# Performance work log

Measured on AMD Instinct MI355X. Metric: run time of the kernel, lower is better.

Reference implementation:

```python
import jax, jax.numpy as jnp
import numpy as np

N_HEADS = 8

def setup_inputs() -> dict:
    key = jax.random.key(0)
    ks = jax.random.split(key, 7)
    B, S, D = 4, 2048, 512
    s = 1.0 / np.sqrt(D)
    return {
        "input_Q": jax.random.normal(ks[0], (B, S, D), jnp.float32),
        "input_K": jax.random.normal(ks[1], (B, S, D), jnp.float32),
        "input_V": jax.random.normal(ks[2], (B, S, D), jnp.float32),
        "W_Q": jax.random.normal(ks[3], (D, D), jnp.float32) * s,
        "W_K": jax.random.normal(ks[4], (D, D), jnp.float32) * s,
        "W_V": jax.random.normal(ks[5], (D, D), jnp.float32) * s,
        "W_O": jax.random.normal(ks[6], (D, D), jnp.float32) * s,
    }

def reference(input_Q, input_K, input_V, W_Q, W_K, W_V, W_O):
    B, Sq, D = input_Q.shape
    Sk = input_K.shape[1]
    H = N_HEADS
    d_k = D // H
    # torch nn.Linear(bias=False): y = x @ W.T
    def proj(x, W):
        return (x @ W.T).reshape(B, -1, H, d_k).transpose(0, 2, 1, 3)  # [B,H,S,dk]
    Q = proj(input_Q, W_Q)
    K = proj(input_K, W_K)
    V = proj(input_V, W_V)
    scale = 1.0 / jnp.sqrt(jnp.float32(d_k))
    scores = jnp.einsum("bhqd,bhkd->bhqk", Q, K) * scale  # [B,H,Sq,Sk]
    # TriangularCausalMask: mask strict upper triangle with -inf
    causal = jnp.tril(jnp.ones((Sq, Sk), dtype=bool))
    scores = jnp.where(causal[None, None], scores, -jnp.inf)
    attn = jax.nn.softmax(scores, axis=-1)
    context = jnp.einsum("bhqk,bhkd->bhqd", attn, V)
    context = context.transpose(0, 2, 1, 3).reshape(B, Sq, D)
    return context @ W_O.T
```

## Files before the change

### kernel.cpp

```cpp
#include <hip/hip_runtime.h>
#include <hip/hip_bf16.h>
#include <math.h>

#define B_  4
#define S_  2048
#define D_  512
#define H_  8
#define DK_ 64
#define M_  (B_ * S_)

using bf16   = __bf16;
using bf16x4 = __bf16 __attribute__((ext_vector_type(4)));
using bf16x8 = __bf16 __attribute__((ext_vector_type(8)));
using f32x4  = float __attribute__((ext_vector_type(4)));

#define MFMA16(a, b, c) __builtin_amdgcn_mfma_f32_16x16x32_bf16((a), (b), (c), 0, 0, 0)
#define EXP2(x) exp2f(x)

typedef __attribute__((address_space(3))) void       lds_void;
typedef const __attribute__((address_space(1))) void gbl_void;

__device__ __forceinline__ void async16(const bf16* g, bf16* lds) {
    __builtin_amdgcn_global_load_lds((gbl_void*)g, (lds_void*)lds, 16, 0, 0);
}

__device__ __forceinline__ bf16x8 ldg8(const bf16* p) {
    return *reinterpret_cast<const bf16x8*>(p);
}

__device__ __forceinline__ size_t fragbase(int g, int k0, int kk, int t) {
    return ((((size_t)(g * 8 + k0) * 2 + kk) * 4 + t) * 64) * 8;
}

__global__ __launch_bounds__(256) void cvt_all(
    const float* __restrict__ x0, const float* __restrict__ x1, const float* __restrict__ x2,
    const float* __restrict__ w0, const float* __restrict__ w1,
    const float* __restrict__ w2, const float* __restrict__ w3,
    bf16* __restrict__ dst)
{
    const int w    = blockIdx.x * 4 + (threadIdx.x >> 6);
    const int lane = threadIdx.x & 63;
    const int lg = lane >> 4, lc = lane & 15;
    const float* src;
    int c;
    size_t dbase;
    if (w < 24576) {
        const int seg = w >> 13;
        c = w & 8191;
        src = (seg == 0) ? x0 : (seg == 1) ? x1 : x2;
        dbase = (size_t)seg << 22;
    } else {
        const int jj = w - 24576;
        const int seg = jj >> 9;
        c = jj & 511;
        src = (seg == 0) ? w0 : (seg == 1) ? w1 : (seg == 2) ? w2 : w3;
        dbase = ((size_t)3 << 22) + ((size_t)seg << 18);
    }
    const int g = c >> 6, k0 = (c >> 3) & 7, kk = (c >> 2) & 1, t = c & 3;
    const size_t soff = ((size_t)(g * 64 + t * 16 + lc) << 9) + k0 * 64 + kk * 32 + lg * 8;
    f32x4 a = *reinterpret_cast<const f32x4*>(src + soff);
    f32x4 b = *reinterpret_cast<const f32x4*>(src + soff + 4);
    bf16x8 r;
    #pragma unroll
    for (int j = 0; j < 4; ++j) { r[j] = (bf16)a[j]; r[j + 4] = (bf16)b[j]; }
    *reinterpret_cast<bf16x8*>(dst + dbase + ((size_t)c << 9) + (size_t)lane * 8) = r;
}

__global__ __launch_bounds__(256) void gemm_qkv(
    const bf16* __restrict__ Xf, const bf16* __restrict__ Wf,
    bf16* __restrict__ qkv)
{
    const int bx  = blockIdx.x;
    const int xcd = bx & 7;
    const int idx = bx >> 3;
    const int mt  = xcd + 8 * (idx & 7);
    const int rest = idx >> 3;
    const int nt  = rest & 3;
    const int z   = rest >> 2;

    const bf16* Xz = Xf + (size_t)z * M_ * D_;
    const bf16* Wz = Wf + (size_t)z * D_ * D_;
    const bool vz = (z == 2);
    const bf16* A  = vz ? Xz : Wz;
    const bf16* Bm = vz ? Wz : Xz;

    const int lane = threadIdx.x & 63;
    const int wave = threadIdx.x >> 6;
    const int lc = lane & 15;
    const int lg = lane >> 4;
    const int gA = (vz ? 2 * mt : 2 * nt) + (wave >> 1);
    const int gB = (vz ? 2 * nt : 2 * mt) + (wave & 1);

    f32x4 acc[4][4] = {};

    #pragma unroll
    for (int k0 = 0; k0 < 8; ++k0) {
        #pragma unroll
        for (int kk = 0; kk < 2; ++kk) {
            bf16x8 af[4], bfm[4];
            #pragma unroll
            for (int t = 0; t < 4; ++t)
                af[t] = ldg8(A + fragbase(gA, k0, kk, t) + (size_t)lane * 8);
            #pragma unroll
            for (int t = 0; t < 4; ++t)
                bfm[t] = ldg8(Bm + fragbase(gB, k0, kk, t) + (size_t)lane * 8);
            #pragma unroll
            for (int mi = 0; mi < 4; ++mi)
                #pragma unroll
                for (int ni = 0; ni < 4; ++ni)
                    acc[mi][ni] = MFMA16(af[mi], bfm[ni], acc[mi][ni]);
        }
    }

    if (z < 2) {
        bf16* Y = qkv + (size_t)z * M_ * D_;
        const float sc = (z == 0) ? 0.125f * 1.4426950408889634f : 1.0f;
        #pragma unroll
        for (int mi = 0; mi < 4; ++mi)
            #pragma unroll
            for (int ni = 0; ni < 4; ++ni) {
                const int d = gA * 64 + mi * 16 + lg * 4;
                const int s = gB * 64 + ni * 16 + lc;
                bf16x4 v;
                #pragma unroll
                for (int r = 0; r < 4; ++r) v[r] = (bf16)(acc[mi][ni][r] * sc);
                const size_t oidx =
                    ((((size_t)(s >> 11) * H_ + (d >> 6)) * S_
                      + (s & (S_ - 1))) << 6) + (d & 63);
                *reinterpret_cast<bf16x4*>(&Y[oidx]) = v;
            }
    } else {
        bf16* Y = qkv + (size_t)2 * M_ * D_;
        #pragma unroll
        for (int mi = 0; mi < 4; ++mi)
            #pragma unroll
            for (int ni = 0; ni < 4; ++ni) {
                const int s = gA * 64 + mi * 16 + lg * 4;
                const int d = gB * 64 + ni * 16 + lc;
                bf16x4 v;
                #pragma unroll
                for (int r = 0; r < 4; ++r) v[r] = (bf16)acc[mi][ni][r];
                const size_t oidx =
                    ((((size_t)(s >> 11)) * H_ + (d >> 6)) << 17)
                    + (size_t)(d & 63) * S_ + (s & (S_ - 1));
                *reinterpret_cast<bf16x4*>(&Y[oidx]) = v;
            }
    }
}

__global__ __launch_bounds__(256) void gemm_out(
    const bf16* __restrict__ CtxF, const bf16* __restrict__ WoF,
    float* __restrict__ out)
{
    const int bx  = blockIdx.x;
    const int xcd = bx & 7;
    const int idx = bx >> 3;
    const int mt  = xcd + 8 * (idx & 15);
    const int nt  = idx >> 4;

    const int lane = threadIdx.x & 63;
    const int wave = threadIdx.x >> 6;
    const int lc = lane & 15;
    const int lg = lane >> 4;
    const int gA = 2 * nt + (wave >> 1);
    const int tA = (wave & 1) * 2;
    const int gB = mt;

    f32x4 acc[2][4] = {};

    #pragma unroll
    for (int k0 = 0; k0 < 8; ++k0) {
        #pragma unroll
        for (int kk = 0; kk < 2; ++kk) {
            bf16x8 af[2], bfm[4];
            #pragma unroll
            for (int ai = 0; ai < 2; ++ai)
                af[ai] = ldg8(WoF + fragbase(gA, k0, kk, tA + ai) + (size_t)lane * 8);
            #pragma unroll
            for (int t = 0; t < 4; ++t)
                bfm[t] = ldg8(CtxF + fragbase(gB, k0, kk, t) + (size_t)lane * 8);
            #pragma unroll
            for (int ai = 0; ai < 2; ++ai)
                #pragma unroll
                for (int ni = 0; ni < 4; ++ni)
                    acc[ai][ni] = MFMA16(af[ai], bfm[ni], acc[ai][ni]);
        }
    }

    #pragma unroll
    for (int ai = 0; ai < 2; ++ai)
        #pragma unroll
        for (int ni = 0; ni < 4; ++ni) {
            const int d = gA * 64 + (tA + ai) * 16 + lg * 4;
            const int s = gB * 64 + ni * 16 + lc;
            *reinterpret_cast<f32x4*>(&out[(size_t)s * D_ + d]) = acc[ai][ni];
        }
}

__device__ __forceinline__ bf16x8 pfrag(const f32x4 a, const f32x4 b) {
    union U4 { bf16x4 v; unsigned int u[2]; };
    U4 pa, pb;
    #pragma unroll
    for (int r = 0; r < 4; ++r) { pa.v[r] = (bf16)a[r]; pb.v[r] = (bf16)b[r]; }
    auto r0 = __builtin_amdgcn_permlane16_swap(pa.u[0], pb.u[0], false, false);
    auto r1 = __builtin_amdgcn_permlane16_swap(pa.u[1], pb.u[1], false, false);
    union U8 { unsigned int u[4]; bf16x8 v; } out;
    out.u[0] = r0[0]; out.u[1] = r1[0]; out.u[2] = r0[1]; out.u[3] = r1[1];
    return out.v;
}

__global__ __launch_bounds__(256) void attn(
    const bf16* __restrict__ QKV, bf16* __restrict__ CtxF)
{
    const int bx = blockIdx.x;
    const int bh = (bx & 7) * 4 + ((bx >> 3) & 3);
    const int pi = bx >> 5;
    const int b = bh >> 3, h = bh & 7;
    const size_t plane = (size_t)S_ * DK_;
    const bf16* Q  = QKV + (size_t)bh * plane;
    const bf16* Kp = QKV + (size_t)(B_ * H_) * plane + (size_t)bh * plane;
    const bf16* Vt = QKV + 2 * (size_t)(B_ * H_) * plane + (size_t)bh * plane;

    const int lane = threadIdx.x & 63;
    const int wave = threadIdx.x >> 6;
    const int lc = lane & 15;
    const int lg = lane >> 4;
    const int sg = ((lg & 1) << 1) | (lg >> 1);
    const int srow = wave * 16 + lc;
    const int mrow = wave * 16 + lc;

    __shared__ bf16 Ks[2][64 * 64];
    __shared__ bf16 Vs[2][64 * 64];

    const int lo = pi;
    const int hi = 31 - pi;

    const int qL = lo * 64 + mrow;
    const int qH = hi * 64 + mrow;
    bf16x8 qfL0 = ldg8(Q + (size_t)qL * DK_ + lg * 8);
    bf16x8 qfL1 = ldg8(Q + (size_t)qL * DK_ + 32 + lg * 8);
    bf16x8 qfH0 = ldg8(Q + (size_t)qH * DK_ + lg * 8);
    bf16x8 qfH1 = ldg8(Q + (size_t)qH * DK_ + 32 + lg * 8);

    f32x4 accL[4] = {}, accH[4] = {};
    float liL = 0.f, liH = 0.f;

    #pragma unroll
    for (int i = 0; i < 2; ++i) {
        const int kc  = i * 4 + lg;
        const int kcv = i * 4 + sg;
        async16(Kp + (size_t)srow * DK_ + kc * 8,  Ks[0] + (i * 256 + wave * 64) * 8);
        async16(Vt + (size_t)srow * S_  + kcv * 8, Vs[0] + (i * 256 + wave * 64) * 8);
    }

    for (int j = 0; j <= hi; ++j) {
        __syncthreads();
        if (j < hi) {
            const int kn = (j + 1) * 64;
            bf16* kd = Ks[(j + 1) & 1];
            bf16* vd = Vs[(j + 1) & 1];
            #pragma unroll
            for (int i = 0; i < 2; ++i) {
                const int kc  = i * 4 + lg;
                const int kcv = i * 4 + sg;
                async16(Kp + (size_t)(kn + srow) * DK_ + kc * 8,
                        kd + (i * 256 + wave * 64) * 8);
                async16(Vt + (size_t)srow * S_ + kn + kcv * 8,
                        vd + (i * 256 + wave * 64) * 8);
            }
        }
        const bf16* ks = Ks[j & 1];
        const bf16* vs = Vs[j & 1];

        bf16x8 kf0[4], kf1[4], vf0[4], vf1[4];
        #pragma unroll
        for (int t = 0; t < 4; ++t) {
            kf0[t] = ldg8(&ks[(t * 64 + lane) * 8]);
            kf1[t] = ldg8(&ks[(256 + t * 64 + lane) * 8]);
            vf0[t] = ldg8(&vs[(t * 64 + lane) * 8]);
            vf1[t] = ldg8(&vs[(256 + t * 64 + lane) * 8]);
        }

        auto step = [&](const bf16x8& qf0, const bf16x8& qf1, bool diag,
                        f32x4* accO, float& li) {
            f32x4 st[4];
            #pragma unroll
            for (int t = 0; t < 4; ++t) {
                f32x4 zz = {};
                zz = MFMA16(kf0[t], qf0, zz);
                st[t] = MFMA16(kf1[t], qf1, zz);
            }
            float rs = 0.f;
            if (diag) {
                #pragma unroll
                for (int t = 0; t < 4; ++t)
                    #pragma unroll
                    for (int r = 0; r < 4; ++r) {
                        const int kl = t * 16 + lg * 4 + r;
                        const float pv = EXP2((kl <= mrow) ? st[t][r] : -1e30f);
                        st[t][r] = pv;
                        rs += pv;
                    }
            } else {
                #pragma unroll
                for (int t = 0; t < 4; ++t)
                    #pragma unroll
                    for (int r = 0; r < 4; ++r) {
                        const float pv = EXP2(st[t][r]);
                        st[t][r] = pv;
                        rs += pv;
                    }
            }
            li += rs;

            const bf16x8 p0 = pfrag(st[0], st[1]);
            const bf16x8 p1 = pfrag(st[2], st[3]);

            #pragma unroll
            for (int t = 0; t < 4; ++t) {
                accO[t] = MFMA16(vf0[t], p0, accO[t]);
                accO[t] = MFMA16(vf1[t], p1, accO[t]);
            }
        };

        step(qfH0, qfH1, j == hi, accH, liH);
        if (j <= lo) step(qfL0, qfL1, j == lo, accL, liL);
    }

    liL += __shfl_xor(liL, 16); liL += __shfl_xor(liL, 32);
    liH += __shfl_xor(liH, 16); liH += __shfl_xor(liH, 32);
    const float rlL = 1.0f / liL;
    const float rlH = 1.0f / liH;
    __syncthreads();
    bf16* T = &Ks[0][0] + wave * 1280;

    #pragma unroll
    for (int half = 0; half < 2; ++half) {
        const f32x4* accO = half ? accH : accL;
        const float rl = half ? rlH : rlL;
        const int jq = half ? hi : lo;
        #pragma unroll
        for (int t = 0; t < 4; ++t) {
            bf16x4 ov;
            #pragma unroll
            for (int r = 0; r < 4; ++r) ov[r] = (bf16)(accO[t][r] * rl);
            *reinterpret_cast<bf16x4*>(&T[lc * 72 + t * 16 + lg * 4]) = ov;
        }
        #pragma unroll
        for (int kk = 0; kk < 2; ++kk) {
            bf16x8 o8 = ldg8(&T[lc * 72 + kk * 32 + lg * 8]);
            *reinterpret_cast<bf16x8*>(
                &CtxF[fragbase(b * 32 + jq, h, kk, wave) + (size_t)lane * 8]) = o8;
        }
    }
}

extern "C" void kernel_launch(void* const* d_in, const int* in_sizes, int n_in,
                              void* d_out, int out_size, void* d_ws, size_t ws_size,
                              hipStream_t stream)
{
    float* out = (float*)d_out;

    bf16* Xf   = (bf16*)d_ws;
    bf16* Wf   = Xf + (size_t)3 * M_ * D_;
    bf16* qkv  = Wf + (size_t)4 * D_ * D_;
    bf16* ctxF = qkv + (size_t)3 * M_ * D_;

    cvt_all<<<6656, 256, 0, stream>>>(
        (const float*)d_in[0], (const float*)d_in[1], (const float*)d_in[2],
        (const float*)d_in[3], (const float*)d_in[4], (const float*)d_in[5],
        (const float*)d_in[6], Xf);

    gemm_qkv<<<dim3(768), 256, 0, stream>>>(Xf, Wf, qkv);
    attn<<<dim3(512), 256, 0, stream>>>(qkv, ctxF);
    gemm_out<<<dim3(512), 256, 0, stream>>>(ctxF, Wf + (size_t)3 * D_ * D_, out);
}
```

Measured before the change: 182.5 us.

## Split paired causal query tiles into one tile per block, doubling grid

```diff
diff --git a/kernel.cpp b/kernel.cpp
--- a/kernel.cpp
+++ b/kernel.cpp
@@ -214,7 +214,7 @@
 {
     const int bx = blockIdx.x;
     const int bh = (bx & 7) * 4 + ((bx >> 3) & 3);
-    const int pi = bx >> 5;
+    const int q  = bx >> 5;
     const int b = bh >> 3, h = bh & 7;
     const size_t plane = (size_t)S_ * DK_;
     const bf16* Q  = QKV + (size_t)bh * plane;
@@ -232,18 +232,12 @@
     __shared__ bf16 Ks[2][64 * 64];
     __shared__ bf16 Vs[2][64 * 64];
 
-    const int lo = pi;
-    const int hi = 31 - pi;
-
-    const int qL = lo * 64 + mrow;
-    const int qH = hi * 64 + mrow;
-    bf16x8 qfL0 = ldg8(Q + (size_t)qL * DK_ + lg * 8);
-    bf16x8 qfL1 = ldg8(Q + (size_t)qL * DK_ + 32 + lg * 8);
-    bf16x8 qfH0 = ldg8(Q + (size_t)qH * DK_ + lg * 8);
-    bf16x8 qfH1 = ldg8(Q + (size_t)qH * DK_ + 32 + lg * 8);
-
-    f32x4 accL[4] = {}, accH[4] = {};
-    float liL = 0.f, liH = 0.f;
+    const int qR = q * 64 + mrow;
+    bf16x8 qf0 = ldg8(Q + (size_t)qR * DK_ + lg * 8);
+    bf16x8 qf1 = ldg8(Q + (size_t)qR * DK_ + 32 + lg * 8);
+
+    f32x4 accO[4] = {};
+    float li = 0.f;
 
     #pragma unroll
     for (int i = 0; i < 2; ++i) {
@@ -253,9 +247,9 @@
         async16(Vt + (size_t)srow * S_  + kcv * 8, Vs[0] + (i * 256 + wave * 64) * 8);
     }
 
-    for (int j = 0; j <= hi; ++j) {
+    for (int j = 0; j <= q; ++j) {
         __syncthreads();
-        if (j < hi) {
+        if (j < q) {
             const int kn = (j + 1) * 64;
             bf16* kd = Ks[(j + 1) & 1];
             bf16* vd = Vs[(j + 1) & 1];
@@ -281,77 +275,63 @@
             vf1[t] = ldg8(&vs[(256 + t * 64 + lane) * 8]);
         }
 
-        auto step = [&](const bf16x8& qf0, const bf16x8& qf1, bool diag,
-                        f32x4* accO, float& li) {
-            f32x4 st[4];
-            #pragma unroll
-            for (int t = 0; t < 4; ++t) {
-                f32x4 zz = {};
-                zz = MFMA16(kf0[t], qf0, zz);
-                st[t] = MFMA16(kf1[t], qf1, zz);
-            }
-            float rs = 0.f;
-            if (diag) {
-                #pragma unroll
-                for (int t = 0; t < 4; ++t)
-                    #pragma unroll
-                    for (int r = 0; r < 4; ++r) {
-                        const int kl = t * 16 + lg * 4 + r;
-                        const float pv = EXP2((kl <= mrow) ? st[t][r] : -1e30f);
-                        st[t][r] = pv;
-                        rs += pv;
-                    }
-            } else {
-                #pragma unroll
-                for (int t = 0; t < 4; ++t)
-                    #pragma unroll
-                    for (int r = 0; r < 4; ++r) {
-                        const float pv = EXP2(st[t][r]);
-                        st[t][r] = pv;
-                        rs += pv;
-                    }
-            }
-            li += rs;
-
-            const bf16x8 p0 = pfrag(st[0], st[1]);
-            const bf16x8 p1 = pfrag(st[2], st[3]);
-
-            #pragma unroll
-            for (int t = 0; t < 4; ++t) {
-                accO[t] = MFMA16(vf0[t], p0, accO[t]);
-                accO[t] = MFMA16(vf1[t], p1, accO[t]);
-            }
-        };
-
-        step(qfH0, qfH1, j == hi, accH, liH);
-        if (j <= lo) step(qfL0, qfL1, j == lo, accL, liL);
-    }
-
-    liL += __shfl_xor(liL, 16); liL += __shfl_xor(liL, 32);
-    liH += __shfl_xor(liH, 16); liH += __shfl_xor(liH, 32);
-    const float rlL = 1.0f / liL;
-    const float rlH = 1.0f / liH;
+        f32x4 st[4];
+        #pragma unroll
+        for (int t = 0; t < 4; ++t) {
+            f32x4 zz = {};
+            zz = MFMA16(kf0[t], qf0, zz);
+            st[t] = MFMA16(kf1[t], qf1, zz);
+        }
+        float rs = 0.f;
+        if (j == q) {
+            #pragma unroll
+            for (int t = 0; t < 4; ++t)
+                #pragma unroll
+                for (int r = 0; r < 4; ++r) {
+                    const int kl = t * 16 + lg * 4 + r;
+                    const float pv = EXP2((kl <= mrow) ? st[t][r] : -1e30f);
+                    st[t][r] = pv;
+                    rs += pv;
+                }
+        } else {
+            #pragma unroll
+            for (int t = 0; t < 4; ++t)
+                #pragma unroll
+                for (int r = 0; r < 4; ++r) {
+                    const float pv = EXP2(st[t][r]);
+                    st[t][r] = pv;
+                    rs += pv;
+                }
+        }
+        li += rs;
+
+        const bf16x8 p0 = pfrag(st[0], st[1]);
+        const bf16x8 p1 = pfrag(st[2], st[3]);
+
+        #pragma unroll
+        for (int t = 0; t < 4; ++t) {
+            accO[t] = MFMA16(vf0[t], p0, accO[t]);
+            accO[t] = MFMA16(vf1[t], p1, accO[t]);
+        }
+    }
+
+    li += __shfl_xor(li, 16); li += __shfl_xor(li, 32);
+    const float rl = 1.0f / li;
     __syncthreads();
     bf16* T = &Ks[0][0] + wave * 1280;
 
     #pragma unroll
-    for (int half = 0; half < 2; ++half) {
-        const f32x4* accO = half ? accH : accL;
-        const float rl = half ? rlH : rlL;
-        const int jq = half ? hi : lo;
-        #pragma unroll
-        for (int t = 0; t < 4; ++t) {
-            bf16x4 ov;
-            #pragma unroll
-            for (int r = 0; r < 4; ++r) ov[r] = (bf16)(accO[t][r] * rl);
-            *reinterpret_cast<bf16x4*>(&T[lc * 72 + t * 16 + lg * 4]) = ov;
-        }
-        #pragma unroll
-        for (int kk = 0; kk < 2; ++kk) {
-            bf16x8 o8 = ldg8(&T[lc * 72 + kk * 32 + lg * 8]);
-            *reinterpret_cast<bf16x8*>(
-                &CtxF[fragbase(b * 32 + jq, h, kk, wave) + (size_t)lane * 8]) = o8;
-        }
+    for (int t = 0; t < 4; ++t) {
+        bf16x4 ov;
+        #pragma unroll
+        for (int r = 0; r < 4; ++r) ov[r] = (bf16)(accO[t][r] * rl);
+        *reinterpret_cast<bf16x4*>(&T[lc * 72 + t * 16 + lg * 4]) = ov;
+    }
+    #pragma unroll
+    for (int kk = 0; kk < 2; ++kk) {
+        bf16x8 o8 = ldg8(&T[lc * 72 + kk * 32 + lg * 8]);
+        *reinterpret_cast<bf16x8*>(
+            &CtxF[fragbase(b * 32 + q, h, kk, wave) + (size_t)lane * 8]) = o8;
     }
 }
 
@@ -372,6 +352,6 @@
         (const float*)d_in[6], Xf);
 
     gemm_qkv<<<dim3(768), 256, 0, stream>>>(Xf, Wf, qkv);
-    attn<<<dim3(512), 256, 0, stream>>>(qkv, ctxF);
+    attn<<<dim3(1024), 256, 0, stream>>>(qkv, ctxF);
     gemm_out<<<dim3(512), 256, 0, stream>>>(ctxF, Wf + (size_t)3 * D_ * D_, out);
 }
```

After: 189.5 us. +3.8%, slower.
